# Optimization experiments

Measured on AMD Instinct MI355X. Metric: run time of the kernel, lower is better.

Reference implementation:

```python
import jax, jax.numpy as jnp
import numpy as np

HEADS = 8
HID = 256
D = HID // HEADS
NEG_SLOPE = 0.2  # PyG leaky_relu negative_slope default in HANConv
NA, NPAP, CIN = 10000, 20000, 256
E = 256000
OUT = 16


def seg_softmax(scores, seg, num_segments):
    # scores: [E, H]; softmax over edges sharing the same dst segment id
    m = jax.ops.segment_max(scores, seg, num_segments=num_segments)
    m = jnp.where(jnp.isfinite(m), m, 0.0)
    e = jnp.exp(scores - m[seg])
    s = jax.ops.segment_sum(e, seg, num_segments=num_segments)
    return e / (s[seg] + 1e-16)


def han_edge(h_src, h_dst, att_src, att_dst, src, dst, num_dst):
    # h_src: [Ns, H, D]; att_*: [H, D]; src/dst: [E]
    a = (h_src * att_src).sum(-1)[src] + (h_dst * att_dst).sum(-1)[dst]  # [E, H]
    alpha = seg_softmax(jax.nn.leaky_relu(a, NEG_SLOPE), dst, num_dst)
    out = jax.ops.segment_sum(h_src[src] * alpha[..., None], dst, num_segments=num_dst)
    return jax.nn.relu(out.reshape(num_dst, HID))


def semantic_group(xs, q, k_W, k_b):
    out = jnp.stack(xs)                                            # [M, N, F]
    score = (jnp.tanh(out @ k_W + k_b) * q).sum(-1).mean(axis=1)   # [M]
    attn = jax.nn.softmax(score)                                   # softmax over metapaths
    return (out * attn[:, None, None]).sum(0)                      # [N, F]


def setup_inputs() -> dict:
    key = jax.random.key(0)
    ks = jax.random.split(key, 32)
    n = lambda i, shape, s: jax.random.normal(ks[i], shape, dtype=jnp.float32) * s
    ri = lambda i, hi: jax.random.randint(ks[i], (E,), 0, hi).astype(jnp.int64)
    w_scale = (1.0 / CIN) ** 0.5
    return {
        "x_author": n(0, (NA, CIN), 1.0),
        "x_paper": n(1, (NPAP, CIN), 1.0),
        "W_author": n(2, (CIN, HID), w_scale),
        "b_author": jnp.zeros((HID,), jnp.float32),
        "W_paper": n(3, (CIN, HID), w_scale),
        "b_paper": jnp.zeros((HID,), jnp.float32),
        "att_sw": n(4, (HEADS, D), 0.1),
        "att_dw": n(5, (HEADS, D), 0.1),
        "att_sc": n(6, (HEADS, D), 0.1),
        "att_dc": n(7, (HEADS, D), 0.1),
        "att_sr": n(8, (HEADS, D), 0.1),
        "att_dr": n(9, (HEADS, D), 0.1),
        "k_W": n(10, (HID, HID), (1.0 / HID) ** 0.5),
        "k_b": jnp.zeros((HID,), jnp.float32),
        "q": n(11, (HID,), 0.1),
        "lin_W": n(12, (HID, OUT), (1.0 / HID) ** 0.5),
        "lin_b": jnp.zeros((OUT,), jnp.float32),
        "ew_src": ri(13, NA), "ew_dst": ri(14, NPAP),
        "ec_src": ri(15, NPAP), "ec_dst": ri(16, NPAP),
        "er_src": ri(17, NPAP), "er_dst": ri(18, NA),
    }


def reference(x_author, x_paper, W_author, b_author, W_paper, b_paper,
              att_sw, att_dw, att_sc, att_dc, att_sr, att_dr,
              k_W, k_b, q, lin_W, lin_b,
              ew_src, ew_dst, ec_src, ec_dst, er_src, er_dst):
    # per-node-type projection -> [N, H, D]
    h_a = (x_author @ W_author + b_author).reshape(NA, HEADS, D)
    h_p = (x_paper @ W_paper + b_paper).reshape(NPAP, HEADS, D)
    # per-edge-type gather / attention / segment-softmax / scatter
    o_writes = han_edge(h_a, h_p, att_sw, att_dw, ew_src, ew_dst, NPAP)  # author->paper
    o_cites = han_edge(h_p, h_p, att_sc, att_dc, ec_src, ec_dst, NPAP)   # paper->paper
    o_rev = han_edge(h_p, h_a, att_sr, att_dr, er_src, er_dst, NA)       # paper->author
    # semantic-level attention over metapaths per dst node type
    paper_out = semantic_group([o_writes, o_cites], q, k_W, k_b)
    author_out = semantic_group([o_rev], q, k_W, k_b)
    # global_add_pool per node type (batch=None -> single graph) + shared linear
    pooled = jnp.stack([author_out.sum(0), paper_out.sum(0)])  # [2, HID]
    return pooled @ lin_W + lin_b                              # [2, OUT]
```

## Files before the change

kernel.cpp:

```cpp
#include <hip/hip_runtime.h>
#include <hip/hip_bf16.h>

#define HEADS 8
#define HID 256
#define NA 10000
#define NPAP 20000
#define NE 256000
#define N_SEG (2 * NPAP + NA)
#define TOTE (3 * NE)
#define NEG_SLOPE 0.2f
#define NBA 157
#define NBP 313
#define PROJ_BLKS (NBA + NBP)
#define DEG_BLKS 3000
#define NATT_BLKS (NPAP + NA)
#define NBS ((N_SEG + 255) / 256)

typedef __attribute__((ext_vector_type(8))) short bf16x8;
typedef __attribute__((ext_vector_type(4))) float f32x4;

__device__ __forceinline__ short f2bf(float x) {
    unsigned u = __float_as_uint(x);
    unsigned r = (u + 0x7fffu + ((u >> 16) & 1u)) >> 16;
    return (short)r;
}
__device__ __forceinline__ float bf2f(short s) {
    return __uint_as_float(((unsigned)(unsigned short)s) << 16);
}

__global__ __launch_bounds__(256) void wconv(
    const float* __restrict__ W_a, short* __restrict__ WaT,
    const float* __restrict__ W_p, short* __restrict__ WpT,
    const float* __restrict__ k_W, short* __restrict__ kWT)
{
    __shared__ short T[64][65];
    int b = blockIdx.x;
    int t = threadIdx.x;
    int z = b >> 4, rem = b & 15;
    int k0 = (rem & 3) * 64, c0 = (rem >> 2) * 64;
    const float* W = z == 0 ? W_a : (z == 1 ? W_p : k_W);
    short* Wt      = z == 0 ? WaT : (z == 1 ? WpT : kWT);
    int rr = t >> 6, c = t & 63;
#pragma unroll
    for (int p = 0; p < 16; ++p) {
        int r = rr + p * 4;
        T[c][r] = f2bf(W[(size_t)(k0 + r) * 256 + c0 + c]);
    }
    __syncthreads();
#pragma unroll
    for (int p = 0; p < 16; ++p) {
        int cc = rr + p * 4;
        Wt[(size_t)(c0 + cc) * 256 + k0 + c] = T[cc][c];
    }
}

__global__ __launch_bounds__(256) void proj_deg(
    const float* __restrict__ A0, const short* __restrict__ Wt0, const float* __restrict__ b0,
    short* __restrict__ C0, unsigned char* __restrict__ H80,
    const float* __restrict__ A1, const short* __restrict__ Wt1, const float* __restrict__ b1,
    short* __restrict__ C1, unsigned char* __restrict__ H81,
    const int* __restrict__ ewd, const int* __restrict__ ecd, const int* __restrict__ erd,
    int* __restrict__ deg4, unsigned short* __restrict__ rank16)
{
    __shared__ short As[64][64];
    __shared__ short Ws[256][64];

    int b = blockIdx.x;
    int t = threadIdx.x;

    if (b >= PROJ_BLKS) {
        int bb = b - PROJ_BLKS;
        int e = bb * 256 + t;
        if (e >= TOTE) return;
        int d;
        if (e < NE)          d = ewd[e];
        else if (e < 2 * NE) d = ecd[e - NE] + NPAP;
        else                 d = erd[e - 2 * NE] + 2 * NPAP;
        int r = atomicAdd(&deg4[(bb & 3) * N_SEG + d], 1);
        rank16[e] = (unsigned short)r;
        return;
    }

    const float* A; const short* Wt; const float* bias; short* Cb; unsigned char* H8; int N, row0;
    if (b < NBA) { A = A0; Wt = Wt0; bias = b0; Cb = C0; H8 = H80; N = NA;   row0 = b * 64; }
    else         { A = A1; Wt = Wt1; bias = b1; Cb = C1; H8 = H81; N = NPAP; row0 = (b - NBA) * 64; }

    int w = t >> 6, l = t & 63;
    int lr = l & 15, lh = l >> 4;
    int swz = (l & 7) << 3;

    f32x4 acc[4][4] = {};

    for (int k0 = 0; k0 < 256; k0 += 64) {
#pragma unroll
        for (int i = 0; i < 4; ++i) {
            int lin = t + i * 256;
            int r = lin >> 4, fc = (lin & 15) << 2;
            float4 v = make_float4(0.f, 0.f, 0.f, 0.f);
            int gr = row0 + r;
            if (gr < N) v = *reinterpret_cast<const float4*>(&A[(size_t)gr * 256 + k0 + fc]);
            short4 o;
            o.x = f2bf(v.x); o.y = f2bf(v.y); o.z = f2bf(v.z); o.w = f2bf(v.w);
            *reinterpret_cast<short4*>(&As[r][fc ^ ((r & 7) << 3)]) = o;
        }
#pragma unroll
        for (int i = 0; i < 8; ++i) {
            int lin = t + i * 256;
            int c = lin >> 3, kc = (lin & 7) << 3;
            *reinterpret_cast<bf16x8*>(&Ws[c][kc ^ ((c & 7) << 3)]) =
                *reinterpret_cast<const bf16x8*>(&Wt[(size_t)c * 256 + k0 + kc]);
        }
        __syncthreads();
#pragma unroll
        for (int kk = 0; kk < 64; kk += 32) {
            int krow = (kk + lh * 8) ^ swz;
            bf16x8 af[4], bfr[4];
#pragma unroll
            for (int mi = 0; mi < 4; ++mi)
                af[mi] = *reinterpret_cast<bf16x8*>(&As[mi * 16 + lr][krow]);
#pragma unroll
            for (int ni = 0; ni < 4; ++ni)
                bfr[ni] = *reinterpret_cast<bf16x8*>(&Ws[w * 64 + ni * 16 + lr][krow]);
#pragma unroll
            for (int mi = 0; mi < 4; ++mi)
#pragma unroll
                for (int ni = 0; ni < 4; ++ni)
                    acc[mi][ni] = __builtin_amdgcn_mfma_f32_16x16x32_bf16(
                        af[mi], bfr[ni], acc[mi][ni], 0, 0, 0);
        }
        __syncthreads();
    }

#pragma unroll
    for (int mi = 0; mi < 4; ++mi) {
        int rb = row0 + mi * 16 + lh * 4;
#pragma unroll
        for (int ni = 0; ni < 4; ++ni) {
            int c = w * 64 + ni * 16 + lr;
            float bc = bias[c];
#pragma unroll
            for (int j = 0; j < 4; ++j) {
                if (rb + j < N) {
                    float v = acc[mi][ni][j] + bc;
                    Cb[(size_t)(rb + j) * 256 + c] = f2bf(v);
                    unsigned pk = __builtin_amdgcn_cvt_pk_fp8_f32(v, v, 0, false);
                    H8[(size_t)(rb + j) * 256 + c] = (unsigned char)pk;
                }
            }
        }
    }
}

__global__ __launch_bounds__(256) void natt_scan(
    const short* __restrict__ h_p, const short* __restrict__ h_a,
    const float* __restrict__ att_dw, const float* __restrict__ att_sc,
    const float* __restrict__ att_dc, const float* __restrict__ att_sr,
    const float* __restrict__ att_sw, const float* __restrict__ att_dr,
    float* __restrict__ a_dw, float* __restrict__ a_sc,
    float* __restrict__ a_dc, float* __restrict__ a_sr,
    float* __restrict__ a_sw, float* __restrict__ a_dr,
    const int* __restrict__ deg4, int* __restrict__ excl, int* __restrict__ bsum)
{
    int b = blockIdx.x;
    int t = threadIdx.x;

    if (b >= NATT_BLKS) {
        __shared__ int buf[256];
        int bb = b - NATT_BLKS;
        int idx = bb * 256 + t;
        int v = 0;
        if (idx < N_SEG)
            v = deg4[idx] + deg4[N_SEG + idx] + deg4[2 * N_SEG + idx] + deg4[3 * N_SEG + idx];
        buf[t] = v;
        __syncthreads();
        for (int off = 1; off < 256; off <<= 1) {
            int add = (t >= off) ? buf[t - off] : 0;
            __syncthreads();
            buf[t] += add;
            __syncthreads();
        }
        if (idx < N_SEG) excl[idx] = buf[t] - v;
        if (t == 255) bsum[bb] = buf[255];
        return;
    }

    if (b < NPAP) {
        float v = bf2f(h_p[(size_t)b * 256 + t]);
        float d0 = v * att_dw[t], d1 = v * att_sc[t], d2 = v * att_dc[t], d3 = v * att_sr[t];
#pragma unroll
        for (int k = 16; k > 0; k >>= 1) {
            d0 += __shfl_xor(d0, k, 64);
            d1 += __shfl_xor(d1, k, 64);
            d2 += __shfl_xor(d2, k, 64);
            d3 += __shfl_xor(d3, k, 64);
        }
        if ((t & 31) == 0) {
            int hh = t >> 5;
            a_dw[b * 8 + hh] = d0; a_sc[b * 8 + hh] = d1;
            a_dc[b * 8 + hh] = d2; a_sr[b * 8 + hh] = d3;
        }
    } else {
        int m = b - NPAP;
        float v = bf2f(h_a[(size_t)m * 256 + t]);
        float d0 = v * att_sw[t], d1 = v * att_dr[t];
#pragma unroll
        for (int k = 16; k > 0; k >>= 1) {
            d0 += __shfl_xor(d0, k, 64);
            d1 += __shfl_xor(d1, k, 64);
        }
        if ((t & 31) == 0) {
            int hh = t >> 5;
            a_sw[m * 8 + hh] = d0; a_dr[m * 8 + hh] = d1;
        }
    }
}

__global__ void scan_l2(const int* __restrict__ bsum, int* __restrict__ boff, int nb)
{
    __shared__ int buf[256];
    int t = threadIdx.x;
    int v = (t < nb) ? bsum[t] : 0;
    buf[t] = v;
    __syncthreads();
    for (int off = 1; off < 256; off <<= 1) {
        int add = (t >= off) ? buf[t - off] : 0;
        __syncthreads();
        buf[t] += add;
        __syncthreads();
    }
    if (t < nb) boff[t] = buf[t] - v;
}

__global__ void scan_l3(const int* __restrict__ excl, const int* __restrict__ boff,
                        const int* __restrict__ deg4,
                        int* __restrict__ starts, int* __restrict__ base4, int N)
{
    int i = blockIdx.x * 256 + threadIdx.x;
    if (i > N) return;
    int v = (i == N) ? TOTE : excl[i] + boff[i >> 8];
    starts[i] = v;
    if (i < N) {
        int c = v;
        base4[i] = c;                 c += deg4[i];
        base4[N_SEG + i] = c;         c += deg4[N_SEG + i];
        base4[2 * N_SEG + i] = c;     c += deg4[2 * N_SEG + i];
        base4[3 * N_SEG + i] = c;
    }
}

__global__ __launch_bounds__(256) void scatter_edges(
    const int* __restrict__ ews, const int* __restrict__ ewd,
    const int* __restrict__ ecs, const int* __restrict__ ecd,
    const int* __restrict__ ers, const int* __restrict__ erd,
    const int* __restrict__ base4, const unsigned short* __restrict__ rank16,
    int* __restrict__ ssrc)
{
    int e = blockIdx.x * 256 + threadIdx.x;
    if (e >= TOTE) return;
    int s, d;
    if (e < NE)          { s = ews[e];          d = ewd[e]; }
    else if (e < 2 * NE) { s = ecs[e - NE];     d = ecd[e - NE] + NPAP; }
    else                 { s = ers[e - 2 * NE]; d = erd[e - 2 * NE] + 2 * NPAP; }
    int shadow = (e >> 8) & 3;
    int pos = base4[shadow * N_SEG + d] + (int)rank16[e];
    ssrc[pos] = s;
}

__global__ __launch_bounds__(256) void han_seg(
    const int* __restrict__ starts, const int* __restrict__ ssrc,
    const float* __restrict__ a_sw, const float* __restrict__ a_dw,
    const float* __restrict__ a_sc, const float* __restrict__ a_dc,
    const float* __restrict__ a_sr, const float* __restrict__ a_dr,
    const unsigned* __restrict__ h8_a, const unsigned* __restrict__ h8_p,
    short* __restrict__ outall)
{
    int w = threadIdx.x >> 6, lane = threadIdx.x & 63;
    int n = blockIdx.x * 4 + w;
    if (n >= N_SEG) return;

    const float* asrc; const float* adst; const unsigned* h8;
    int nloc;
    if (n < NPAP)          { nloc = n;            asrc = a_sw; adst = a_dw; h8 = h8_a; }
    else if (n < 2 * NPAP) { nloc = n - NPAP;     asrc = a_sc; adst = a_dc; h8 = h8_p; }
    else                   { nloc = n - 2 * NPAP; asrc = a_sr; adst = a_dr; h8 = h8_p; }

    int hh = lane >> 3;
    int c0 = lane << 2;
    float ad = adst[nloc * 8 + hh];

    int i = starts[n], end = starts[n + 1];
    float ac0 = 0.f, ac1 = 0.f, ac2 = 0.f, ac3 = 0.f, ps = 0.f;

    for (; i + 4 <= end; i += 4) {
        int s0 = __builtin_amdgcn_readfirstlane(ssrc[i]);
        int s1 = __builtin_amdgcn_readfirstlane(ssrc[i + 1]);
        int s2 = __builtin_amdgcn_readfirstlane(ssrc[i + 2]);
        int s3 = __builtin_amdgcn_readfirstlane(ssrc[i + 3]);
        float x0 = asrc[s0 * 8 + hh] + ad;
        float x1 = asrc[s1 * 8 + hh] + ad;
        float x2 = asrc[s2 * 8 + hh] + ad;
        float x3 = asrc[s3 * 8 + hh] + ad;
        unsigned v0 = h8[s0 * 64 + lane];
        unsigned v1 = h8[s1 * 64 + lane];
        unsigned v2 = h8[s2 * 64 + lane];
        unsigned v3 = h8[s3 * 64 + lane];
        x0 = x0 > 0.f ? x0 : NEG_SLOPE * x0;
        x1 = x1 > 0.f ? x1 : NEG_SLOPE * x1;
        x2 = x2 > 0.f ? x2 : NEG_SLOPE * x2;
        x3 = x3 > 0.f ? x3 : NEG_SLOPE * x3;
        float e0 = __expf(x0), e1 = __expf(x1), e2 = __expf(x2), e3 = __expf(x3);
        ps += (e0 + e1) + (e2 + e3);
        ac0 += e0 * __builtin_amdgcn_cvt_f32_fp8(v0, 0) + e1 * __builtin_amdgcn_cvt_f32_fp8(v1, 0)
             + e2 * __builtin_amdgcn_cvt_f32_fp8(v2, 0) + e3 * __builtin_amdgcn_cvt_f32_fp8(v3, 0);
        ac1 += e0 * __builtin_amdgcn_cvt_f32_fp8(v0, 1) + e1 * __builtin_amdgcn_cvt_f32_fp8(v1, 1)
             + e2 * __builtin_amdgcn_cvt_f32_fp8(v2, 1) + e3 * __builtin_amdgcn_cvt_f32_fp8(v3, 1);
        ac2 += e0 * __builtin_amdgcn_cvt_f32_fp8(v0, 2) + e1 * __builtin_amdgcn_cvt_f32_fp8(v1, 2)
             + e2 * __builtin_amdgcn_cvt_f32_fp8(v2, 2) + e3 * __builtin_amdgcn_cvt_f32_fp8(v3, 2);
        ac3 += e0 * __builtin_amdgcn_cvt_f32_fp8(v0, 3) + e1 * __builtin_amdgcn_cvt_f32_fp8(v1, 3)
             + e2 * __builtin_amdgcn_cvt_f32_fp8(v2, 3) + e3 * __builtin_amdgcn_cvt_f32_fp8(v3, 3);
    }
    for (; i < end; ++i) {
        int s0 = __builtin_amdgcn_readfirstlane(ssrc[i]);
        float x0 = asrc[s0 * 8 + hh] + ad;
        unsigned v0 = h8[s0 * 64 + lane];
        x0 = x0 > 0.f ? x0 : NEG_SLOPE * x0;
        float e0 = __expf(x0);
        ps += e0;
        ac0 += e0 * __builtin_amdgcn_cvt_f32_fp8(v0, 0);
        ac1 += e0 * __builtin_amdgcn_cvt_f32_fp8(v0, 1);
        ac2 += e0 * __builtin_amdgcn_cvt_f32_fp8(v0, 2);
        ac3 += e0 * __builtin_amdgcn_cvt_f32_fp8(v0, 3);
    }

    float inv = 1.0f / (ps + 1e-16f);
    float o0 = ac0 * inv, o1 = ac1 * inv, o2 = ac2 * inv, o3 = ac3 * inv;
    short4 o;
    o.x = f2bf(o0 > 0.f ? o0 : 0.f);
    o.y = f2bf(o1 > 0.f ? o1 : 0.f);
    o.z = f2bf(o2 > 0.f ? o2 : 0.f);
    o.w = f2bf(o3 > 0.f ? o3 : 0.f);
    *reinterpret_cast<short4*>(&outall[(size_t)n * 256 + c0]) = o;
}

__global__ void colsum3(const short* __restrict__ outall,
                        float* __restrict__ cw, float* __restrict__ cc,
                        float* __restrict__ cr)
{
    int t = threadIdx.x;
    int r0 = blockIdx.x * 32;
    int rend = r0 + 32 < N_SEG ? r0 + 32 : N_SEG;
    float s = 0.f;
    for (int r = r0; r < rend; ++r) s += bf2f(outall[(size_t)r * 256 + t]);
    float* cs = r0 < NPAP ? cw : (r0 < 2 * NPAP ? cc : cr);
    atomicAdd(&cs[t], s);
}

__global__ __launch_bounds__(256) void gemm_score(
    const short* __restrict__ A0, const short* __restrict__ Wt, const float* __restrict__ kb,
    float* __restrict__ sAcc0, int N0, int nb0,
    const short* __restrict__ A1, float* __restrict__ sAcc1, int N1,
    const float* __restrict__ q)
{
    __shared__ short As[64][64];
    __shared__ short Ws[256][64];
    __shared__ float red[256];

    int bx = blockIdx.x;
    const short* A; float* sAcc; int N, row0;
    if (bx < nb0) { A = A0; sAcc = sAcc0; N = N0; row0 = bx * 64; }
    else          { A = A1; sAcc = sAcc1; N = N1; row0 = (bx - nb0) * 64; }

    int tid = threadIdx.x;
    int w = tid >> 6, l = tid & 63;
    int lr = l & 15, lh = l >> 4;
    int swz = (l & 7) << 3;

    f32x4 acc[4][4] = {};

    for (int k0 = 0; k0 < 256; k0 += 64) {
#pragma unroll
        for (int i = 0; i < 2; ++i) {
            int lin = tid + i * 256;
            int r = lin >> 3, kc = (lin & 7) << 3;
            bf16x8 v = {};
            int gr = row0 + r;
            if (gr < N) v = *reinterpret_cast<const bf16x8*>(&A[(size_t)gr * 256 + k0 + kc]);
            *reinterpret_cast<bf16x8*>(&As[r][kc ^ ((r & 7) << 3)]) = v;
        }
#pragma unroll
        for (int i = 0; i < 8; ++i) {
            int lin = tid + i * 256;
            int c = lin >> 3, kc = (lin & 7) << 3;
            *reinterpret_cast<bf16x8*>(&Ws[c][kc ^ ((c & 7) << 3)]) =
                *reinterpret_cast<const bf16x8*>(&Wt[(size_t)c * 256 + k0 + kc]);
        }
        __syncthreads();
#pragma unroll
        for (int kk = 0; kk < 64; kk += 32) {
            int krow = (kk + lh * 8) ^ swz;
            bf16x8 af[4], bfr[4];
#pragma unroll
            for (int mi = 0; mi < 4; ++mi)
                af[mi] = *reinterpret_cast<bf16x8*>(&As[mi * 16 + lr][krow]);
#pragma unroll
            for (int ni = 0; ni < 4; ++ni)
                bfr[ni] = *reinterpret_cast<bf16x8*>(&Ws[w * 64 + ni * 16 + lr][krow]);
#pragma unroll
            for (int mi = 0; mi < 4; ++mi)
#pragma unroll
                for (int ni = 0; ni < 4; ++ni)
                    acc[mi][ni] = __builtin_amdgcn_mfma_f32_16x16x32_bf16(
                        af[mi], bfr[ni], acc[mi][ni], 0, 0, 0);
        }
        __syncthreads();
    }

    float s = 0.f;
#pragma unroll
    for (int mi = 0; mi < 4; ++mi) {
        int rb = row0 + mi * 16 + lh * 4;
#pragma unroll
        for (int ni = 0; ni < 4; ++ni) {
            int c = w * 64 + ni * 16 + lr;
            float bc = kb[c], qc = q[c];
#pragma unroll
            for (int j = 0; j < 4; ++j) {
                if (rb + j < N) s += tanhf(acc[mi][ni][j] + bc) * qc;
            }
        }
    }
    red[tid] = s;
    __syncthreads();
    for (int k = 128; k > 0; k >>= 1) {
        if (tid < k) red[tid] += red[tid + k];
        __syncthreads();
    }
    if (tid == 0) atomicAdd(sAcc, red[0]);
}

__global__ void finalize(const float* __restrict__ scoreAcc,
                         const float* __restrict__ colsum_w, const float* __restrict__ colsum_c,
                         const float* __restrict__ colsum_r,
                         const float* __restrict__ lin_W, const float* __restrict__ lin_b,
                         float* __restrict__ out)
{
    int t = threadIdx.x;
    if (t >= 32) return;
    float sw = scoreAcc[0] / (float)NPAP;
    float scs = scoreAcc[1] / (float)NPAP;
    float mx = fmaxf(sw, scs);
    float ew = expf(sw - mx), ec = expf(scs - mx);
    float aw = ew / (ew + ec), ac = ec / (ew + ec);
    int row = t >> 4, j = t & 15;
    float acc = lin_b[j];
    for (int c = 0; c < 256; ++c) {
        float p = (row == 0) ? colsum_r[c] : (aw * colsum_w[c] + ac * colsum_c[c]);
        acc += p * lin_W[c * 16 + j];
    }
    out[row * 16 + j] = acc;
}

extern "C" void kernel_launch(void* const* d_in, const int* in_sizes, int n_in,
                              void* d_out, int out_size, void* d_ws, size_t ws_size,
                              hipStream_t stream)
{
    const float* x_a   = (const float*)d_in[0];
    const float* x_p   = (const float*)d_in[1];
    const float* W_a   = (const float*)d_in[2];
    const float* b_a   = (const float*)d_in[3];
    const float* W_p   = (const float*)d_in[4];
    const float* b_p   = (const float*)d_in[5];
    const float* att_sw = (const float*)d_in[6];
    const float* att_dw = (const float*)d_in[7];
    const float* att_sc = (const float*)d_in[8];
    const float* att_dc = (const float*)d_in[9];
    const float* att_sr = (const float*)d_in[10];
    const float* att_dr = (const float*)d_in[11];
    const float* k_W   = (const float*)d_in[12];
    const float* k_b   = (const float*)d_in[13];
    const float* q     = (const float*)d_in[14];
    const float* lin_W = (const float*)d_in[15];
    const float* lin_b = (const float*)d_in[16];
    const int* ew_src = (const int*)d_in[17];
    const int* ew_dst = (const int*)d_in[18];
    const int* ec_src = (const int*)d_in[19];
    const int* ec_dst = (const int*)d_in[20];
    const int* er_src = (const int*)d_in[21];
    const int* er_dst = (const int*)d_in[22];

    float* ws = (float*)d_ws;
    size_t off = 0;
    auto align4 = [&]() { off = (off + 3) & ~(size_t)3; };

    short* h_a_bf = (short*)(ws + off); off += (size_t)NA * HID / 2;
    short* h_p_bf = (short*)(ws + off); off += (size_t)NPAP * HID / 2;
    unsigned char* h8_a = (unsigned char*)(ws + off); off += (size_t)NA * HID / 4;
    unsigned char* h8_p = (unsigned char*)(ws + off); off += (size_t)NPAP * HID / 4;
    short* WaT  = (short*)(ws + off); off += 256 * 256 / 2;
    short* WpT  = (short*)(ws + off); off += 256 * 256 / 2;
    short* kWT  = (short*)(ws + off); off += 256 * 256 / 2;
    float* a_sw = ws + off; off += (size_t)NA * 8;
    float* a_dw = ws + off; off += (size_t)NPAP * 8;
    float* a_sc = ws + off; off += (size_t)NPAP * 8;
    float* a_dc = ws + off; off += (size_t)NPAP * 8;
    float* a_sr = ws + off; off += (size_t)NPAP * 8;
    float* a_dr = ws + off; off += (size_t)NA * 8;
    short* outall = (short*)(ws + off); off += (size_t)N_SEG * HID / 2;
    int* starts  = (int*)(ws + off); off += N_SEG + 1; align4();
    int* base4   = (int*)(ws + off); off += 4 * N_SEG; align4();
    int* sexcl   = (int*)(ws + off); off += N_SEG + 1; align4();
    int* sbsum   = (int*)(ws + off); off += 256;
    int* sboff   = (int*)(ws + off); off += 256;
    int* ssrc    = (int*)(ws + off); off += TOTE;
    unsigned short* rank16 = (unsigned short*)(ws + off); off += TOTE / 2;
    size_t zero_start = off;
    int* deg4       = (int*)(ws + off); off += 4 * N_SEG; align4();
    float* colsum_w = ws + off; off += 256;
    float* colsum_c = ws + off; off += 256;
    float* colsum_r = ws + off; off += 256;
    float* score    = ws + off; off += 2;
    size_t zero_bytes = (off - zero_start) * sizeof(float);

    hipMemsetAsync(ws + zero_start, 0, zero_bytes, stream);

    wconv<<<48, 256, 0, stream>>>(W_a, WaT, W_p, WpT, k_W, kWT);

    proj_deg<<<PROJ_BLKS + DEG_BLKS, 256, 0, stream>>>(
        x_a, WaT, b_a, h_a_bf, h8_a,
        x_p, WpT, b_p, h_p_bf, h8_p,
        ew_dst, ec_dst, er_dst, deg4, rank16);

    natt_scan<<<NATT_BLKS + NBS, 256, 0, stream>>>(
        h_p_bf, h_a_bf, att_dw, att_sc, att_dc, att_sr, att_sw, att_dr,
        a_dw, a_sc, a_dc, a_sr, a_sw, a_dr,
        deg4, sexcl, sbsum);

    scan_l2<<<1, 256, 0, stream>>>(sbsum, sboff, NBS);
    scan_l3<<<(N_SEG + 1 + 255) / 256, 256, 0, stream>>>(sexcl, sboff, deg4, starts, base4, N_SEG);

    scatter_edges<<<(TOTE + 255) / 256, 256, 0, stream>>>(ew_src, ew_dst, ec_src, ec_dst,
                                                          er_src, er_dst, base4, rank16, ssrc);

    han_seg<<<(N_SEG + 3) / 4, 256, 0, stream>>>(starts, ssrc, a_sw, a_dw, a_sc, a_dc, a_sr, a_dr,
                                                 (const unsigned*)h8_a, (const unsigned*)h8_p,
                                                 outall);

    colsum3<<<(N_SEG + 31) / 32, 256, 0, stream>>>(outall, colsum_w, colsum_c, colsum_r);
    gemm_score<<<2 * NBP, 256, 0, stream>>>(
        outall, kWT, k_b, score + 0, NPAP, NBP,
        outall + (size_t)NPAP * HID, score + 1, NPAP, q);

    finalize<<<1, 64, 0, stream>>>(score, colsum_w, colsum_c, colsum_r, lin_W, lin_b, (float*)d_out);
}
```

Measured before the change: 230.4 us.

## Merge scan kernels, batch edge scatter, coarsen colsum, use fast tanh

Fuses the two-level scan kernels into one launch in which every block redoes the small block-offset scan in shared memory, removing one launch and the global offset buffer. The edge scatter now handles two edges per thread, and colsum works on 128-row blocks that accumulate into the per-type sums separately, which means fewer blocks and fewer atomics. The score epilogue swaps tanhf for an exp/rcp approximation clamped to ±15. These trade redundant scan work per block and slightly lower tanh accuracy for less launch overhead and less atomic traffic.

```diff
diff --git a/kernel.cpp b/kernel.cpp
--- a/kernel.cpp
+++ b/kernel.cpp
@@ -27,6 +27,11 @@
 __device__ __forceinline__ float bf2f(short s) {
     return __uint_as_float(((unsigned)(unsigned short)s) << 16);
 }
+__device__ __forceinline__ float ftanh(float x) {
+    float xc = fminf(fmaxf(x, -15.f), 15.f);
+    float e = __expf(2.f * xc);
+    return 1.f - 2.f * __builtin_amdgcn_rcpf(e + 1.f);
+}
 
 __global__ __launch_bounds__(256) void wconv(
     const float* __restrict__ W_a, short* __restrict__ WaT,
@@ -215,11 +220,15 @@
     }
 }
 
-__global__ void scan_l2(const int* __restrict__ bsum, int* __restrict__ boff, int nb)
+__global__ __launch_bounds__(256) void scan_l23(
+    const int* __restrict__ excl, const int* __restrict__ bsum,
+    const int* __restrict__ deg4,
+    int* __restrict__ starts, int* __restrict__ base4, int N)
 {
     __shared__ int buf[256];
+    __shared__ int boff_s[256];
     int t = threadIdx.x;
-    int v = (t < nb) ? bsum[t] : 0;
+    int v = (t < NBS) ? bsum[t] : 0;
     buf[t] = v;
     __syncthreads();
     for (int off = 1; off < 256; off <<= 1) {
@@ -228,19 +237,15 @@
         buf[t] += add;
         __syncthreads();
     }
-    if (t < nb) boff[t] = buf[t] - v;
-}
-
-__global__ void scan_l3(const int* __restrict__ excl, const int* __restrict__ boff,
-                        const int* __restrict__ deg4,
-                        int* __restrict__ starts, int* __restrict__ base4, int N)
-{
-    int i = blockIdx.x * 256 + threadIdx.x;
+    boff_s[t] = buf[t] - v;
+    __syncthreads();
+
+    int i = blockIdx.x * 256 + t;
     if (i > N) return;
-    int v = (i == N) ? TOTE : excl[i] + boff[i >> 8];
-    starts[i] = v;
+    int val = (i == N) ? TOTE : excl[i] + boff_s[i >> 8];
+    starts[i] = val;
     if (i < N) {
-        int c = v;
+        int c = val;
         base4[i] = c;                 c += deg4[i];
         base4[N_SEG + i] = c;         c += deg4[N_SEG + i];
         base4[2 * N_SEG + i] = c;     c += deg4[2 * N_SEG + i];
@@ -255,15 +260,21 @@
     const int* __restrict__ base4, const unsigned short* __restrict__ rank16,
     int* __restrict__ ssrc)
 {
-    int e = blockIdx.x * 256 + threadIdx.x;
-    if (e >= TOTE) return;
-    int s, d;
-    if (e < NE)          { s = ews[e];          d = ewd[e]; }
-    else if (e < 2 * NE) { s = ecs[e - NE];     d = ecd[e - NE] + NPAP; }
-    else                 { s = ers[e - 2 * NE]; d = erd[e - 2 * NE] + 2 * NPAP; }
-    int shadow = (e >> 8) & 3;
-    int pos = base4[shadow * N_SEG + d] + (int)rank16[e];
-    ssrc[pos] = s;
+    int base = blockIdx.x * 512 + threadIdx.x;
+    int ss[2], pos[2];
+#pragma unroll
+    for (int j = 0; j < 2; ++j) {
+        int e = base + j * 256;
+        int s, d;
+        if (e < NE)          { s = ews[e];          d = ewd[e]; }
+        else if (e < 2 * NE) { s = ecs[e - NE];     d = ecd[e - NE] + NPAP; }
+        else                 { s = ers[e - 2 * NE]; d = erd[e - 2 * NE] + 2 * NPAP; }
+        int shadow = (e >> 8) & 3;
+        ss[j] = s;
+        pos[j] = base4[shadow * N_SEG + d] + (int)rank16[e];
+    }
+#pragma unroll
+    for (int j = 0; j < 2; ++j) ssrc[pos[j]] = ss[j];
 }
 
 __global__ __launch_bounds__(256) void han_seg(
@@ -347,12 +358,18 @@
                         float* __restrict__ cr)
 {
     int t = threadIdx.x;
-    int r0 = blockIdx.x * 32;
-    int rend = r0 + 32 < N_SEG ? r0 + 32 : N_SEG;
-    float s = 0.f;
-    for (int r = r0; r < rend; ++r) s += bf2f(outall[(size_t)r * 256 + t]);
-    float* cs = r0 < NPAP ? cw : (r0 < 2 * NPAP ? cc : cr);
-    atomicAdd(&cs[t], s);
+    int r0 = blockIdx.x * 128;
+    int rend = r0 + 128 < N_SEG ? r0 + 128 : N_SEG;
+    float s0 = 0.f, s1 = 0.f, s2 = 0.f;
+    for (int r = r0; r < rend; ++r) {
+        float v = bf2f(outall[(size_t)r * 256 + t]);
+        if (r < NPAP) s0 += v;
+        else if (r < 2 * NPAP) s1 += v;
+        else s2 += v;
+    }
+    if (s0 != 0.f) atomicAdd(&cw[t], s0);
+    if (s1 != 0.f) atomicAdd(&cc[t], s1);
+    if (s2 != 0.f) atomicAdd(&cr[t], s2);
 }
 
 __global__ __launch_bounds__(256) void gemm_score(
@@ -425,7 +442,7 @@
             float bc = kb[c], qc = q[c];
 #pragma unroll
             for (int j = 0; j < 4; ++j) {
-                if (rb + j < N) s += tanhf(acc[mi][ni][j] + bc) * qc;
+                if (rb + j < N) s += ftanh(acc[mi][ni][j] + bc) * qc;
             }
         }
     }
@@ -510,7 +527,6 @@
     int* base4   = (int*)(ws + off); off += 4 * N_SEG; align4();
     int* sexcl   = (int*)(ws + off); off += N_SEG + 1; align4();
     int* sbsum   = (int*)(ws + off); off += 256;
-    int* sboff   = (int*)(ws + off); off += 256;
     int* ssrc    = (int*)(ws + off); off += TOTE;
     unsigned short* rank16 = (unsigned short*)(ws + off); off += TOTE / 2;
     size_t zero_start = off;
@@ -535,17 +551,16 @@
         a_dw, a_sc, a_dc, a_sr, a_sw, a_dr,
         deg4, sexcl, sbsum);
 
-    scan_l2<<<1, 256, 0, stream>>>(sbsum, sboff, NBS);
-    scan_l3<<<(N_SEG + 1 + 255) / 256, 256, 0, stream>>>(sexcl, sboff, deg4, starts, base4, N_SEG);
-
-    scatter_edges<<<(TOTE + 255) / 256, 256, 0, stream>>>(ew_src, ew_dst, ec_src, ec_dst,
-                                                          er_src, er_dst, base4, rank16, ssrc);
+    scan_l23<<<(N_SEG + 1 + 255) / 256, 256, 0, stream>>>(sexcl, sbsum, deg4, starts, base4, N_SEG);
+
+    scatter_edges<<<TOTE / 512, 256, 0, stream>>>(ew_src, ew_dst, ec_src, ec_dst,
+                                                  er_src, er_dst, base4, rank16, ssrc);
 
     han_seg<<<(N_SEG + 3) / 4, 256, 0, stream>>>(starts, ssrc, a_sw, a_dw, a_sc, a_dc, a_sr, a_dr,
                                                  (const unsigned*)h8_a, (const unsigned*)h8_p,
                                                  outall);
 
-    colsum3<<<(N_SEG + 31) / 32, 256, 0, stream>>>(outall, colsum_w, colsum_c, colsum_r);
+    colsum3<<<(N_SEG + 127) / 128, 256, 0, stream>>>(outall, colsum_w, colsum_c, colsum_r);
     gemm_score<<<2 * NBP, 256, 0, stream>>>(
         outall, kWT, k_b, score + 0, NPAP, NBP,
         outall + (size_t)NPAP * HID, score + 1, NPAP, q);
```

Result: slower. 246.0 us (+6.8%).
